# Kernel optimization log

Hardware: AMD Instinct MI355X
Metric: run time of the kernel (lower is better)

## Reference

```python
import jax, jax.numpy as jnp
import numpy as np

DIM = 512
HEADS = 8
DHEAD = DIM // HEADS
M = DIM // 2          # num_landmarks = 256
ITERS = 6             # pinv iterations
KSIZE = 33            # residual conv kernel (seq axis)
EPS = 1e-5            # LayerNorm eps (torch default)


def moore_penrose_pinv(a, iters=ITERS):
    # a: [b, h, m, m]; iterative Newton-Schulz style pseudo-inverse
    abs_a = jnp.abs(a)
    col = abs_a.sum(-1).max()   # global max of row-sums
    row = abs_a.sum(-2).max()   # global max of col-sums
    z = jnp.swapaxes(a, -1, -2) / (col * row)
    I = jnp.eye(a.shape[-1], dtype=a.dtype)

    def body(z, _):
        az = a @ z
        z = 0.25 * z @ (13.0 * I - az @ (15.0 * I - az @ (7.0 * I - az)))
        return z, None

    z, _ = jax.lax.scan(body, z, None, length=iters)
    return z


def res_conv(v, conv_w):
    # v: [b, h, n, d] treated as NCHW (C=heads), depthwise kernel (33, 1)
    return jax.lax.conv_general_dilated(
        v, conv_w, window_strides=(1, 1),
        padding=((KSIZE // 2, KSIZE // 2), (0, 0)),
        dimension_numbers=('NCHW', 'OIHW', 'NCHW'),
        feature_group_count=HEADS)


def setup_inputs() -> dict:
    key = jax.random.key(0)
    ks = jax.random.split(key, 5)
    b, n = 4, 4096  # n % M == 0 -> no padding branch
    x = jax.random.normal(ks[0], (b, n, DIM), jnp.float32)
    norm_w = jnp.ones((DIM,), jnp.float32)
    norm_b = jnp.zeros((DIM,), jnp.float32)
    Wqkv = jax.random.normal(ks[1], (DIM, 3 * DIM), jnp.float32) * (DIM ** -0.5)
    Wout = jax.random.normal(ks[2], (DIM, DIM), jnp.float32) * (DIM ** -0.5)
    bout = jnp.zeros((DIM,), jnp.float32)
    conv_w = jax.random.normal(ks[3], (HEADS, 1, KSIZE, 1), jnp.float32) * 0.05
    return {"x": x, "norm_w": norm_w, "norm_b": norm_b,
            "Wqkv": Wqkv, "Wout": Wout, "bout": bout, "conv_w": conv_w}


def reference(x, norm_w, norm_b, Wqkv, Wout, bout, conv_w):
    b, n, dim = x.shape
    # LayerNorm
    mu = x.mean(-1, keepdims=True)
    var = ((x - mu) ** 2).mean(-1, keepdims=True)
    xn = (x - mu) * jax.lax.rsqrt(var + EPS) * norm_w + norm_b

    # QKV projection, split heads: [b, h, n, d]
    qkv = xn @ Wqkv
    q, k, v = jnp.split(qkv, 3, axis=-1)
    sh = lambda t: t.reshape(b, n, HEADS, DHEAD).transpose(0, 2, 1, 3)
    q, k, v = sh(q), sh(k), sh(v)
    q = q * (DHEAD ** -0.5)

    # landmarks: mean over consecutive segments of length l = n // M
    l = n // M
    q_l = q.reshape(b, HEADS, M, l, DHEAD).mean(3)  # [b,h,m,d]
    k_l = k.reshape(b, HEADS, M, l, DHEAD).mean(3)

    sim1 = jnp.einsum('bhid,bhjd->bhij', q, k_l)    # [b,h,n,m]
    sim2 = jnp.einsum('bhid,bhjd->bhij', q_l, k_l)  # [b,h,m,m]
    sim3 = jnp.einsum('bhid,bhjd->bhij', q_l, k)    # [b,h,m,n]
    a1 = jax.nn.softmax(sim1, axis=-1)
    a2 = jax.nn.softmax(sim2, axis=-1)
    a3 = jax.nn.softmax(sim3, axis=-1)

    a2_inv = moore_penrose_pinv(a2)
    out = (a1 @ a2_inv) @ (a3 @ v)                  # [b,h,n,d]
    out = out + res_conv(v, conv_w)                  # residual depthwise conv on v

    out = out.transpose(0, 2, 1, 3).reshape(b, n, dim)
    out = out @ Wout + bout                          # to_out (dropout = identity in eval)
    return x + out                                   # TransLayer residual
```

## Files before the change

kernel.cpp:

```cpp
#include <hip/hip_runtime.h>
#include <hip/hip_bf16.h>

#define BB 4
#define NN 4096
#define DIMM 512
#define HH 8
#define DD 64
#define MM 256
#define LL 16
#define BHH 32
#define NROW (BB*NN)
#define KS 33

typedef __attribute__((ext_vector_type(8))) short short8;
typedef __attribute__((ext_vector_type(4))) float float4v;

static __device__ __forceinline__ unsigned short bf16_bits(float v) {
    __hip_bfloat16 h = __float2bfloat16(v);
    return *reinterpret_cast<unsigned short*>(&h);
}

static __device__ __forceinline__ void gl_lds16(const void* g, void* l) {
    __builtin_amdgcn_global_load_lds((const __attribute__((address_space(1))) void*)g,
                                     (__attribute__((address_space(3))) void*)l, 16, 0, 0);
}

static __device__ __forceinline__ void bar_nv() {
    asm volatile("s_waitcnt lgkmcnt(0)\ns_barrier" ::: "memory");
}

static __device__ __forceinline__ int xcd_swz(int hw, int nwg) {
    return (hw & 7) * (nwg >> 3) + (hw >> 3);
}

__launch_bounds__(256)
__global__ void ln_kernel(const float* __restrict__ x,
                          const float* __restrict__ w,
                          const float* __restrict__ bvec,
                          __hip_bfloat16* __restrict__ xn) {
    int row = blockIdx.x;
    int t = threadIdx.x;
    const float* xr = x + (long)row * DIMM;
    float v0 = xr[t];
    float v1 = xr[t + 256];
    __shared__ float red[256];
    red[t] = v0 + v1;
    __syncthreads();
    for (int off = 128; off > 0; off >>= 1) { if (t < off) red[t] += red[t + off]; __syncthreads(); }
    float mu = red[0] * (1.0f / DIMM);
    __syncthreads();
    float d0 = v0 - mu, d1 = v1 - mu;
    red[t] = d0 * d0 + d1 * d1;
    __syncthreads();
    for (int off = 128; off > 0; off >>= 1) { if (t < off) red[t] += red[t + off]; __syncthreads(); }
    float var = red[0] * (1.0f / DIMM);
    float rs = rsqrtf(var + 1e-5f);
    xn[(long)row * DIMM + t]       = __float2bfloat16(d0 * rs * w[t]       + bvec[t]);
    xn[(long)row * DIMM + t + 256] = __float2bfloat16(d1 * rs * w[t + 256] + bvec[t + 256]);
}

__launch_bounds__(256)
__global__ void transpose_bf16(const float* __restrict__ in, __hip_bfloat16* __restrict__ outp,
                               int K, int N) {
    __shared__ float tile[32][33];
    int k0 = blockIdx.y * 32, n0 = blockIdx.x * 32;
    int tx = threadIdx.x & 31, ty = threadIdx.x >> 5;
    #pragma unroll
    for (int i = 0; i < 32; i += 8)
        tile[ty + i][tx] = in[(long)(k0 + ty + i) * N + n0 + tx];
    __syncthreads();
    #pragma unroll
    for (int i = 0; i < 32; i += 8)
        outp[(long)(n0 + ty + i) * K + k0 + tx] = __float2bfloat16(tile[tx][ty + i]);
}

enum { EPI_NONE = 0, EPI_QKV = 1, EPI_OUT = 2 };

template<int EPI>
__launch_bounds__(256)
__global__ void gemm_mfma(const __hip_bfloat16* __restrict__ A,
                          const __hip_bfloat16* __restrict__ Bt,
                          float* __restrict__ C, int M, int N, int K,
                          const float* __restrict__ bias,
                          const float* __restrict__ resid,
                          __hip_bfloat16* __restrict__ qb,
                          __hip_bfloat16* __restrict__ kb,
                          __hip_bfloat16* __restrict__ vtb) {
    __shared__ __hip_bfloat16 As[128][64];
    __shared__ __hip_bfloat16 Bs[128][64];
    const int t = threadIdx.x;
    const int hw = blockIdx.y * gridDim.x + blockIdx.x;
    const int lg = xcd_swz(hw, gridDim.x * gridDim.y);
    const int m0 = (lg / gridDim.x) * 128, n0 = (lg % gridDim.x) * 128;
    const int wave = t >> 6, lane = t & 63;
    const int wrow = wave >> 1, wcol = wave & 1;
    const int lm = lane & 15, quad = lane >> 4;
    const int wbase = wave * 64;

    const __hip_bfloat16* gA[4];
    const __hip_bfloat16* gB[4];
    __hip_bfloat16* lA[4];
    __hip_bfloat16* lB[4];
    #pragma unroll
    for (int p = 0; p < 4; ++p) {
        int idx = t + p * 256;
        int r = idx >> 3;
// ... 53 lines not shown
        for (int j = 0; j < 4; ++j) {
            int rowb = m0 + wrow * 64 + i * 16 + quad * 4;
            int col  = n0 + wcol * 64 + j * 16 + lm;
            if (EPI == EPI_QKV) {
                int b = rowb >> 12, seq = rowb & (NN - 1);
                int which = col >> 9, rem = col & 511;
                int h = rem >> 6, dd = rem & 63;
                int bh = b * HH + h;
                if (which == 0) {
                    #pragma unroll
                    for (int r = 0; r < 4; ++r)
                        qb[((long)bh * NN + seq + r) * DD + dd] = __float2bfloat16(acc[i][j][r] * 0.125f);
                } else if (which == 1) {
                    #pragma unroll
                    for (int r = 0; r < 4; ++r)
                        kb[((long)bh * NN + seq + r) * DD + dd] = __float2bfloat16(acc[i][j][r]);
                } else {
                    union { unsigned long long u; unsigned short s[4]; } pk;
                    #pragma unroll
                    for (int r = 0; r < 4; ++r) pk.s[r] = bf16_bits(acc[i][j][r]);
                    *(unsigned long long*)&vtb[((long)bh * DD + dd) * NN + seq] = pk.u;
                }
            } else {
                #pragma unroll
                for (int r = 0; r < 4; ++r) {
                    int row = rowb + r;
                    C[(long)row * N + col] = acc[i][j][r] + bias[col] + resid[(long)row * N + col];
                }
            }
        }
    }
}

__launch_bounds__(256)
__global__ void gemm_pinv(const __hip_bfloat16* __restrict__ A,
                          const __hip_bfloat16* __restrict__ Bt,
                          __hip_bfloat16* __restrict__ CnBf,
                          float* __restrict__ CnF,
                          __hip_bfloat16* __restrict__ CTbf,
                          float diag, float sgn, float scale) {
    __shared__ __hip_bfloat16 As[64][256];
    __shared__ __hip_bfloat16 Bs[64][256];
    const int t = threadIdx.x;
    const int hw = (blockIdx.z * 4 + blockIdx.y) * 4 + blockIdx.x;
    const int lg = xcd_swz(hw, 512);
    const long base = (long)(lg >> 4) << 16;
    const int m0 = ((lg >> 2) & 3) * 64, n0 = (lg & 3) * 64;
    const int wave = t >> 6, lane = t & 63;
    const int wr = wave >> 1, wc = wave & 1;
    const int lm = lane & 15, quad = lane >> 4;
    const __hip_bfloat16* Ab = A + base;
    const __hip_bfloat16* Bb = Bt + base;

    #pragma unroll
    for (int p = 0; p < 8; ++p) {
        int idx = t + p * 256;
        int r = idx >> 5;
        int csrc = ((idx & 31) ^ (r & 7)) * 8;
        int cb = idx * 8;
        gl_lds16(&Ab[(long)(m0 + r) * 256 + csrc], &As[0][0] + cb);
        gl_lds16(&Bb[(long)(n0 + r) * 256 + csrc], &Bs[0][0] + cb);
    }

    const char* pA[2][2];
    const char* pB[2][2];
    #pragma unroll
    for (int i = 0; i < 2; ++i) {
        int ra = wr * 32 + i * 16 + lm;
        int rb = wc * 32 + i * 16 + lm;
        int ca = quad ^ (ra & 3), ra2 = (ra >> 2) & 1;
        int cb2 = quad ^ (rb & 3), rb2 = (rb >> 2) & 1;
        pA[0][i] = (const char*)&As[ra][(4 * ra2       + ca)  * 8];
        pA[1][i] = (const char*)&As[ra][(4 * (1 - ra2) + ca)  * 8];
        pB[0][i] = (const char*)&Bs[rb][(4 * rb2       + cb2) * 8];
        pB[1][i] = (const char*)&Bs[rb][(4 * (1 - rb2) + cb2) * 8];
    }
    __syncthreads();

// ... 4 lines not shown
        #pragma unroll
        for (int i = 0; i < 2; ++i) {
            af[i]  = *(const short8*)(pA[ksu & 1][i] + (ksu >> 1) * 128);
            bfr[i] = *(const short8*)(pB[ksu & 1][i] + (ksu >> 1) * 128);
        }
        #pragma unroll
        for (int i = 0; i < 2; ++i)
            #pragma unroll
            for (int j = 0; j < 2; ++j)
                acc[i][j] = __builtin_amdgcn_mfma_f32_16x16x32_bf16(af[i], bfr[j], acc[i][j], 0, 0, 0);
    }

    #pragma unroll
    for (int i = 0; i < 2; ++i)
        #pragma unroll
        for (int j = 0; j < 2; ++j) {
            const int rowb = wr * 32 + i * 16 + quad * 4;
            const int col  = wc * 32 + j * 16 + lm;
            union { unsigned long long u; unsigned short s[4]; } pk;
            #pragma unroll
            for (int r = 0; r < 4; ++r) {
                float v = acc[i][j][r] * scale;
                long off = base + (long)(m0 + rowb + r) * 256 + n0 + col;
                if (CnBf) CnBf[off] = __float2bfloat16(v);
                if (CnF)  CnF[off]  = v;
                float tv = sgn * v + ((m0 + rowb + r) == (n0 + col) ? diag : 0.0f);
                pk.s[r] = bf16_bits(tv);
            }
            if (CTbf)
                *(unsigned long long*)&CTbf[base + (long)(n0 + col) * 256 + m0 + rowb] = pk.u;
        }
}

__launch_bounds__(256)
__global__ void gemm_pinv2(const __hip_bfloat16* __restrict__ zA,
                           const __hip_bfloat16* __restrict__ pAg,
                           const __hip_bfloat16* __restrict__ t3T,
                           __hip_bfloat16* __restrict__ zOut,
                           float* __restrict__ zF,
                           __hip_bfloat16* __restrict__ pOut,
                           __hip_bfloat16* __restrict__ t1T) {
    __shared__ __hip_bfloat16 As[64][256];
    __shared__ __hip_bfloat16 Bs[64][256];
    const int t = threadIdx.x;
    const int hw = blockIdx.y * 16 + blockIdx.x;
    const int lg = xcd_swz(hw, 1024);
    const int pair = lg >> 5;
    const int half = (lg >> 4) & 1;
    const int tile = lg & 15;
    const long base = (long)pair << 16;
    const int m0 = (tile >> 2) * 64, n0 = (tile & 3) * 64;
    const int wave = t >> 6, lane = t & 63;
    const int wr = wave >> 1, wc = wave & 1;
    const int lm = lane & 15, quad = lane >> 4;
    const __hip_bfloat16* Ab = (half ? pAg : zA) + base;
    const __hip_bfloat16* Bb = t3T + base;

    #pragma unroll
    for (int p = 0; p < 8; ++p) {
        int idx = t + p * 256;
        int r = idx >> 5;
        int csrc = ((idx & 31) ^ (r & 7)) * 8;
        int cb = idx * 8;
        gl_lds16(&Ab[(long)(m0 + r) * 256 + csrc], &As[0][0] + cb);
        gl_lds16(&Bb[(long)(n0 + r) * 256 + csrc], &Bs[0][0] + cb);
    }

    const char* pA[2][2];
    const char* pB[2][2];
    #pragma unroll
    for (int i = 0; i < 2; ++i) {
        int ra = wr * 32 + i * 16 + lm;
        int rb = wc * 32 + i * 16 + lm;
        int ca = quad ^ (ra & 3), ra2 = (ra >> 2) & 1;
        int cb2 = quad ^ (rb & 3), rb2 = (rb >> 2) & 1;
        pA[0][i] = (const char*)&As[ra][(4 * ra2       + ca)  * 8];
// ... 15 lines not shown
        #pragma unroll
        for (int i = 0; i < 2; ++i)
            #pragma unroll
            for (int j = 0; j < 2; ++j)
                acc[i][j] = __builtin_amdgcn_mfma_f32_16x16x32_bf16(af[i], bfr[j], acc[i][j], 0, 0, 0);
    }

    #pragma unroll
    for (int i = 0; i < 2; ++i)
        #pragma unroll
        for (int j = 0; j < 2; ++j) {
            const int rowb = wr * 32 + i * 16 + quad * 4;
            const int col  = wc * 32 + j * 16 + lm;
            union { unsigned long long u; unsigned short s[4]; } pk;
            #pragma unroll
            for (int r = 0; r < 4; ++r) {
                float v = acc[i][j][r] * 0.25f;
                long off = base + (long)(m0 + rowb + r) * 256 + n0 + col;
                if (half == 0) {
                    zOut[off] = __float2bfloat16(v);
                    if (zF) zF[off] = v;
                } else {
                    pOut[off] = __float2bfloat16(v);
                    float tv = -v + ((m0 + rowb + r) == (n0 + col) ? 7.0f : 0.0f);
                    pk.s[r] = bf16_bits(tv);
                }
            }
            if (half)
                *(unsigned long long*)&t1T[base + (long)(n0 + col) * 256 + m0 + rowb] = pk.u;
        }
}

__launch_bounds__(256)
__global__ void pinv_prep(const float* __restrict__ a2, const float* __restrict__ scl,
                          __hip_bfloat16* __restrict__ a2bf, __hip_bfloat16* __restrict__ z0T,
                          __hip_bfloat16* __restrict__ z0n) {
    __shared__ float tl[64][65];
    const int t = threadIdx.x;
    const long base = (long)blockIdx.z << 16;
    const int i0 = blockIdx.y * 64, j0 = blockIdx.x * 64;
    float s = scl[0];
    #pragma unroll
    for (int p = 0; p < 16; ++p) {
        int idx = t + p * 256;
        int r = idx >> 6, c = idx & 63;
        long off = base + (long)(i0 + r) * 256 + j0 + c;
        float v = a2[off];
        a2bf[off] = __float2bfloat16(v);
        float zv = v * s;
        z0T[off] = __float2bfloat16(zv);
        tl[r][c] = zv;
    }
    __syncthreads();
    int r = t & 63;
    #pragma unroll
    for (int u = 0; u < 16; ++u) {
        int c = u * 4 + (t >> 6);
        z0n[base + (long)(j0 + c) * 256 + i0 + r] = __float2bfloat16(tl[r][c]);
    }
}

__launch_bounds__(256)
__global__ void sim2_softmax(const float* __restrict__ q_l, const float* __restrict__ k_l,
                             float* __restrict__ a2) {
    const int t = threadIdx.x;
    const int lg = xcd_swz(blockIdx.x, 128);
    const int bh = lg >> 2;
    const int m0 = (lg & 3) * 64;
    const int tx = t & 15, ty = t >> 4;
    const float* Ab = q_l + (long)bh * MM * DD;
    const float* Bb = k_l + (long)bh * MM * DD;

    __shared__ float As[16][64];
    __shared__ float Bs[16][256];

    float acc[4][16] = {};

    for (int k0 = 0; k0 < DD; k0 += 16) {
        {
            int r = t >> 2, kk4 = (t & 3) * 4;
            float4 va = *(const float4*)(Ab + (long)(m0 + r) * DD + k0 + kk4);
            As[kk4 + 0][r] = va.x; As[kk4 + 1][r] = va.y; As[kk4 + 2][r] = va.z; As[kk4 + 3][r] = va.w;
        }
        {
            #pragma unroll
            for (int g = 0; g < 4; ++g) {
                float4 vb = *(const float4*)(Bb + (long)t * DD + k0 + g * 4);
                Bs[g * 4 + 0][t] = vb.x; Bs[g * 4 + 1][t] = vb.y;
                Bs[g * 4 + 2][t] = vb.z; Bs[g * 4 + 3][t] = vb.w;
            }
        }
        __syncthreads();
        #pragma unroll
        for (int kk = 0; kk < 16; ++kk) {
            float a[4], b[16];
            #pragma unroll
            for (int r2 = 0; r2 < 4; ++r2) a[r2] = As[kk][ty * 4 + r2];
            #pragma unroll
// ... 7 lines not shown
        __syncthreads();
    }

    float* outb = a2 + ((long)bh << 16);
    #pragma unroll
    for (int r2 = 0; r2 < 4; ++r2) {
        float mx = acc[r2][0];
        #pragma unroll
        for (int c = 1; c < 16; ++c) mx = fmaxf(mx, acc[r2][c]);
        mx = fmaxf(mx, __shfl_xor(mx, 1));
        mx = fmaxf(mx, __shfl_xor(mx, 2));
        mx = fmaxf(mx, __shfl_xor(mx, 4));
        mx = fmaxf(mx, __shfl_xor(mx, 8));
        float sum = 0.f;
        #pragma unroll
        for (int c = 0; c < 16; ++c) {
            acc[r2][c] = __expf(acc[r2][c] - mx);
            sum += acc[r2][c];
        }
        sum += __shfl_xor(sum, 1);
        sum += __shfl_xor(sum, 2);
        sum += __shfl_xor(sum, 4);
        sum += __shfl_xor(sum, 8);
        float inv = 1.0f / sum;
        int row = m0 + ty * 4 + r2;
        #pragma unroll
        for (int c = 0; c < 16; ++c)
            outb[(long)row * 256 + tx + 16 * c] = acc[r2][c] * inv;
    }
}

__launch_bounds__(256)
__global__ void gemm64(const float* __restrict__ A, const float* __restrict__ Bm,
                       float* __restrict__ C, __hip_bfloat16* __restrict__ wtT,
                       int M, int N, int K, long sA, long sB, long sC, float alpha) {
    const int gx = gridDim.x, gxy = gridDim.x * gridDim.y;
    const int hw = blockIdx.z * gxy + blockIdx.y * gx + blockIdx.x;
    const int lg = xcd_swz(hw, gxy * gridDim.z);
    const int bz = lg / gxy;
    const int rem = lg % gxy;
    const float* Ab = A + (long)bz * sA;
    const float* Bb = Bm + (long)bz * sB;

    __shared__ float As[16][64];
    __shared__ float Bs[16][64];

    const int tid = threadIdx.x;
    const int tx = tid & 15;
    const int ty = tid >> 4;
    const int m0 = (rem / gx) * 64;
    const int n0 = (rem % gx) * 64;

    float acc[4][4] = {};

    for (int k0 = 0; k0 < K; k0 += 16) {
        {
            int r  = tid >> 2;
            int kk = (tid & 3) * 4;
            float4 va = *(const float4*)(Ab + (long)(m0 + r) * K + k0 + kk);
            As[kk + 0][r] = va.x; As[kk + 1][r] = va.y; As[kk + 2][r] = va.z; As[kk + 3][r] = va.w;
        }
        {
            int kk = tid >> 4;
            int j  = (tid & 15) * 4;
            float4 vb = *(const float4*)(Bb + (long)(k0 + kk) * N + n0 + j);
            Bs[kk][j + 0] = vb.x; Bs[kk][j + 1] = vb.y; Bs[kk][j + 2] = vb.z; Bs[kk][j + 3] = vb.w;
        }
        __syncthreads();
        #pragma unroll
        for (int kk = 0; kk < 16; ++kk) {
            float a0 = As[kk][ty * 4 + 0], a1 = As[kk][ty * 4 + 1];
            float a2 = As[kk][ty * 4 + 2], a3 = As[kk][ty * 4 + 3];
            float b0 = Bs[kk][tx * 4 + 0], b1 = Bs[kk][tx * 4 + 1];
            float b2 = Bs[kk][tx * 4 + 2], b3 = Bs[kk][tx * 4 + 3];
            acc[0][0] += a0 * b0; acc[0][1] += a0 * b1; acc[0][2] += a0 * b2; acc[0][3] += a0 * b3;
            acc[1][0] += a1 * b0; acc[1][1] += a1 * b1; acc[1][2] += a1 * b2; acc[1][3] += a1 * b3;
            acc[2][0] += a2 * b0; acc[2][1] += a2 * b1; acc[2][2] += a2 * b2; acc[2][3] += a2 * b3;
            acc[3][0] += a3 * b0; acc[3][1] += a3 * b1; acc[3][2] += a3 * b2; acc[3][3] += a3 * b3;
        }
        __syncthreads();
    }

    if (wtT) {
        __hip_bfloat16* wb = wtT + (long)bz * DD * MM;
        #pragma unroll
        for (int r = 0; r < 4; ++r)
            #pragma unroll
            for (int c = 0; c < 4; ++c)
                wb[(long)(n0 + tx * 4 + c) * MM + m0 + ty * 4 + r] = __float2bfloat16(acc[r][c] * alpha);
    } else {
        float* Cb = C + (long)bz * sC;
        #pragma unroll
        for (int r = 0; r < 4; ++r)
            #pragma unroll
            for (int c = 0; c < 4; ++c)
                Cb[(long)(m0 + ty * 4 + r) * N + n0 + tx * 4 + c] = acc[r][c] * alpha;
    }
}

__global__ void landmark_kernel(const __hip_bfloat16* __restrict__ qb,
                                const __hip_bfloat16* __restrict__ kb,
                                float* __restrict__ q_l, float* __restrict__ k_l,
                                __hip_bfloat16* __restrict__ q_lb,
                                __hip_bfloat16* __restrict__ k_lb) {
    int bh = blockIdx.x >> 8;
    int m  = blockIdx.x & 255;
    int d  = threadIdx.x;
    const __hip_bfloat16* src = (blockIdx.y ? kb : qb) + ((long)bh * NN + m * LL) * DD + d;
    float s = 0.f;
    #pragma unroll
    for (int t = 0; t < LL; ++t) s += __bfloat162float(src[(long)t * DD]);
    s *= (1.0f / LL);
    long off = ((long)bh * MM + m) * DD + d;
    if (blockIdx.y) { k_l[off] = s; k_lb[off] = __float2bfloat16(s); }
    else            { q_l[off] = s; q_lb[off] = __float2bfloat16(s); }
}

__launch_bounds__(256)
__global__ void redmax_kernel(const float* __restrict__ a2, float* __restrict__ red) {
    int blk = blockIdx.x;
    int bh = blk >> 3, cg = blk & 7;
    int t = threadIdx.x;
    const float* Ab = a2 + ((long)bh << 16) + cg * 32;
    int c = t & 31, rg = t >> 5;
    float s = 0.f;
    for (int r = rg * 32; r < rg * 32 + 32; ++r) s += Ab[(long)r * 256 + c];
    __shared__ float m[256];
    m[t] = s;
    __syncthreads();
    if (t < 32) {
        float cs = 0.f;
        #pragma unroll
        for (int g = 0; g < 8; ++g) cs += m[t + 32 * g];
        m[t] = cs;
    }
    __syncthreads();
    if (t == 0) {
        float mx = m[0];
        #pragma unroll
        for (int i = 1; i < 32; ++i) mx = fmaxf(mx, m[i]);
        red[blk] = mx;
    }
}

__launch_bounds__(256)
__global__ void scale_kernel(const float* __restrict__ red, float* __restrict__ scl) {
    __shared__ float b[256];
    int t = threadIdx.x;
    b[t] = red[t];
    __syncthreads();
    for (int off = 128; off > 0; off >>= 1) {
        if (t < off) b[t] = fmaxf(b[t], b[t + off]);
        __syncthreads();
    }
    if (t == 0) scl[0] = 1.0f / b[0];
}

__launch_bounds__(256)
__global__ void a3v_mfma(const __hip_bfloat16* __restrict__ qlb,
                         const __hip_bfloat16* __restrict__ kb,
                         const __hip_bfloat16* __restrict__ vtb,
                         float* __restrict__ opart, float* __restrict__ lpart) {
    const int hw = blockIdx.y * 16 + blockIdx.x;
    const int lg = xcd_swz(hw, 512);
    const int bh = lg >> 4;
    const int mt = (lg >> 2) & 3;
    const int ns = lg & 3;
    const int t = threadIdx.x;
    const int wave = t >> 6, lane = t & 63;
    const int wr = wave >> 1, wc = wave & 1;
    const int lm = lane & 15, quad = lane >> 4;
    const int r8 = t >> 3, c8 = (t & 7) * 8;

    __shared__ __hip_bfloat16 Qs[64][72];
    __shared__ __hip_bfloat16 Ks[64][72];
    __shared__ __hip_bfloat16 Vt[64][72];
    __shared__ __hip_bfloat16 Ps[64][72];
    __shared__ float lredS[64][2];

    {
        const __hip_bfloat16* qbase = qlb + ((long)bh * MM + mt * 64) * DD;
        *(uint4*)&Qs[r8][c8]      = *(const uint4*)&qbase[(long)r8 * DD + c8];
        *(uint4*)&Qs[r8 + 32][c8] = *(const uint4*)&qbase[(long)(r8 + 32) * DD + c8];
    }

    float4v acc[2][2] = {};
    float lacc[2][4] = {};
    const __hip_bfloat16* kbase = kb + ((long)bh * NN + ns * 1024) * DD;
    const __hip_bfloat16* vbase = vtb + (long)bh * DD * NN + ns * 1024;

    uint4 kv0 = *(const uint4*)&kbase[(long)r8 * DD + c8];
    uint4 kv1 = *(const uint4*)&kbase[(long)(r8 + 32) * DD + c8];
    uint4 vv0 = *(const uint4*)&vbase[(long)r8 * NN + c8];
    uint4 vv1 = *(const uint4*)&vbase[(long)(r8 + 32) * NN + c8];
    bar_nv();

    for (int ch = 0; ch < 16; ++ch) {
        *(uint4*)&Ks[r8][c8]      = kv0;
        *(uint4*)&Ks[r8 + 32][c8] = kv1;
        *(uint4*)&Vt[r8][c8]      = vv0;
        *(uint4*)&Vt[r8 + 32][c8] = vv1;
        if (ch < 15) {
            kv0 = *(const uint4*)&kbase[(long)((ch + 1) * 64 + r8) * DD + c8];
            kv1 = *(const uint4*)&kbase[(long)((ch + 1) * 64 + r8 + 32) * DD + c8];
            vv0 = *(const uint4*)&vbase[(long)r8 * NN + (ch + 1) * 64 + c8];
            vv1 = *(const uint4*)&vbase[(long)(r8 + 32) * NN + (ch + 1) * 64 + c8];
        }
        bar_nv();

        float4v s[2][2] = {};
        #pragma unroll
        for (int ks = 0; ks < 64; ks += 32) {
            short8 af[2], bfr[2];
            #pragma unroll
            for (int i = 0; i < 2; ++i) {
                af[i]  = *(const short8*)&Qs[wr * 32 + i * 16 + lm][ks + quad * 8];
                bfr[i] = *(const short8*)&Ks[wc * 32 + i * 16 + lm][ks + quad * 8];
            }
            #pragma unroll
            for (int i = 0; i < 2; ++i)
                #pragma unroll
                for (int j = 0; j < 2; ++j)
                    s[i][j] = __builtin_amdgcn_mfma_f32_16x16x32_bf16(af[i], bfr[j], s[i][j], 0, 0, 0);
        }
        #pragma unroll
        for (int i = 0; i < 2; ++i)
            #pragma unroll
            for (int j = 0; j < 2; ++j)
                #pragma unroll
                for (int r2 = 0; r2 < 4; ++r2) {
                    float e = __expf(s[i][j][r2]);
                    lacc[i][r2] += e;
                    Ps[wr * 32 + i * 16 + quad * 4 + r2][wc * 32 + j * 16 + lm] = __float2bfloat16(e);
                }
        bar_nv();

        #pragma unroll
        for (int ks = 0; ks < 64; ks += 32) {
            short8 af[2], bfr[2];
            #pragma unroll
            for (int i = 0; i < 2; ++i) {
                af[i]  = *(const short8*)&Ps[wr * 32 + i * 16 + lm][ks + quad * 8];
                bfr[i] = *(const short8*)&Vt[wc * 32 + i * 16 + lm][ks + quad * 8];
            }
            #pragma unroll
            for (int i = 0; i < 2; ++i)
                #pragma unroll
                for (int j = 0; j < 2; ++j)
                    acc[i][j] = __builtin_amdgcn_mfma_f32_16x16x32_bf16(af[i], bfr[j], acc[i][j], 0, 0, 0);
        }
        bar_nv();
    }

    #pragma unroll
    for (int i = 0; i < 2; ++i)
        #pragma unroll
        for (int r2 = 0; r2 < 4; ++r2) {
            float s = lacc[i][r2];
            s += __shfl_xor(s, 1);
            s += __shfl_xor(s, 2);
            s += __shfl_xor(s, 4);
            s += __shfl_xor(s, 8);
            if (lm == 0) lredS[wr * 32 + i * 16 + quad * 4 + r2][wc] = s;
        }
    __syncthreads();
    if (t < 64)
        lpart[((bh * 4 + mt) * 4 + ns) * 64 + t] = lredS[t][0] + lredS[t][1];
    const long pbase = ((long)((bh * 4 + mt) * 4 + ns)) << 12;
    #pragma unroll
    for (int i = 0; i < 2; ++i)
        #pragma unroll
        for (int j = 0; j < 2; ++j)
            #pragma unroll
            for (int r2 = 0; r2 < 4; ++r2)
                opart[pbase + (long)(wr * 32 + i * 16 + quad * 4 + r2) * 64 + wc * 32 + j * 16 + lm] = acc[i][j][r2];
}

__global__ void a3v_combine(const float* __restrict__ opart, const float* __restrict__ lpart,
                            float* __restrict__ a3v) {
    int idx = blockIdx.x * 256 + threadIdx.x;
    int d  = idx & 63;
    int m  = (idx >> 6) & 255;
    int bh = idx >> 14;
    int mt = m >> 6, r = m & 63;
    int pb = (bh * 4 + mt) * 4;
    float osum = 0.f, lsum = 0.f;
    #pragma unroll
    for (int ns = 0; ns < 4; ++ns) {
        osum += opart[(((long)(pb + ns)) << 12) + r * 64 + d];
        lsum += lpart[(pb + ns) * 64 + r];
    }
    a3v[((long)bh * MM + m) * DD + d] = osum / lsum;
}

__launch_bounds__(256)
__global__ void attn_out_mfma(const __hip_bfloat16* __restrict__ qb,
                              const __hip_bfloat16* __restrict__ klb,
                              const __hip_bfloat16* __restrict__ wtb,
                              const __hip_bfloat16* __restrict__ vtb,
                              const float* __restrict__ convw,
                              __hip_bfloat16* __restrict__ ctx) {
    const int hw = blockIdx.y * 64 + blockIdx.x;
    const int lg = xcd_swz(hw, 2048);
    const int bh = lg >> 6;
    const int b = bh >> 3, h = bh & 7;
    const int i0 = (lg & 63) * 64;
    const int t = threadIdx.x;
    const int wave = t >> 6, lane = t & 63;
    const int wr = wave >> 1, wc = wave & 1;
    const int lm = lane & 15, quad = lane >> 4;
    const int r8 = t >> 3, c8 = (t & 7) * 8;

    __shared__ __hip_bfloat16 Qs[64][72];
    __shared__ __hip_bfloat16 KW[2][64][72];
    __shared__ __hip_bfloat16 Ps[64][72];
    __shared__ __hip_bfloat16 Vc[64][104];
    __shared__ float lredS[64][2];
    __shared__ float dsum[64];
    __shared__ float cwS[KS];
    __hip_bfloat16 (*Tpl)[104] = reinterpret_cast<__hip_bfloat16 (*)[104]>(&KW[0][0][0]);

    if (t < KS) cwS[t] = convw[h * KS + t];

    {
        const __hip_bfloat16* qbase = qb + ((long)bh * NN + i0) * DD;
// ... 157 lines not shown
    const float* norm_b = (const float*)d_in[2];
    const float* Wqkv   = (const float*)d_in[3];
    const float* Wout   = (const float*)d_in[4];
    const float* bout   = (const float*)d_in[5];
    const float* conv_w = (const float*)d_in[6];
    float* out = (float*)d_out;

    float* ws = (float*)d_ws;
    size_t o = 0;
    auto alloc = [&](size_t n) { float* p = ws + o; o += n; return p; };
    auto allocb = [&](size_t n) { return (__hip_bfloat16*)alloc((n + 1) / 2); };

    __hip_bfloat16* xn_bf  = allocb((size_t)NROW * DIMM);
    __hip_bfloat16* wqt_bf = allocb((size_t)3 * DIMM * DIMM);
    __hip_bfloat16* wot_bf = allocb((size_t)DIMM * DIMM);
    __hip_bfloat16* ctx_bf = allocb((size_t)NROW * DIMM);
    __hip_bfloat16* q_bf   = allocb((size_t)BHH * NN * DD);
    __hip_bfloat16* k_bf   = allocb((size_t)BHH * NN * DD);
    __hip_bfloat16* vt_bf  = allocb((size_t)BHH * DD * NN);
    __hip_bfloat16* qlb    = allocb((size_t)BHH * MM * DD);
    __hip_bfloat16* klb    = allocb((size_t)BHH * MM * DD);
    __hip_bfloat16* wt_bf  = allocb((size_t)BHH * DD * MM);
    float* q_l  = alloc((size_t)BHH * MM * DD);
    float* k_l  = alloc((size_t)BHH * MM * DD);
    float* a2   = alloc((size_t)BHH * MM * MM);
    float* zb   = alloc((size_t)BHH * MM * MM);
    float* az   = alloc((size_t)BHH * MM * MM);
    float* gb   = alloc((size_t)BHH * MM * MM);
    float* tb   = alloc((size_t)BHH * MM * MM);
    float* z2   = alloc((size_t)BHH * MM * MM);
    float* a3v  = alloc((size_t)BHH * MM * DD);
    float* opart = alloc((size_t)BHH * 4 * 4 * 64 * 64);
    float* lpart = alloc((size_t)BHH * 4 * 4 * 64);
    float* red  = alloc(256);
    float* scl  = alloc(64);

    const size_t HB = 1048576;
    __hip_bfloat16* a2bf = (__hip_bfloat16*)az;
    __hip_bfloat16* z0Tb = (__hip_bfloat16*)(az + HB);
    __hip_bfloat16* zpA  = (__hip_bfloat16*)gb;
    __hip_bfloat16* zpB  = (__hip_bfloat16*)(gb + HB);
    __hip_bfloat16* PnA  = (__hip_bfloat16*)tb;
    __hip_bfloat16* t1A  = (__hip_bfloat16*)(tb + HB);
    __hip_bfloat16* t2T  = (__hip_bfloat16*)z2;
    __hip_bfloat16* t3Tb = (__hip_bfloat16*)(z2 + HB);

    ln_kernel<<<NROW, 256, 0, stream>>>(x, norm_w, norm_b, xn_bf);

    transpose_bf16<<<dim3(3 * DIMM / 32, DIMM / 32), 256, 0, stream>>>(Wqkv, wqt_bf, DIMM, 3 * DIMM);
    transpose_bf16<<<dim3(DIMM / 32, DIMM / 32), 256, 0, stream>>>(Wout, wot_bf, DIMM, DIMM);

    gemm_mfma<EPI_QKV><<<dim3(3 * DIMM / 128, NROW / 128), 256, 0, stream>>>(
        xn_bf, wqt_bf, nullptr, NROW, 3 * DIMM, DIMM,
        nullptr, nullptr, q_bf, k_bf, vt_bf);

    landmark_kernel<<<dim3(BHH * MM, 2), 64, 0, stream>>>(q_bf, k_bf, q_l, k_l, qlb, klb);

    sim2_softmax<<<128, 256, 0, stream>>>(q_l, k_l, a2);

    redmax_kernel<<<BHH * 8, 256, 0, stream>>>(a2, red);
    scale_kernel<<<1, 256, 0, stream>>>(red, scl);

    dim3 g512(4, 4, BHH);
    pinv_prep<<<g512, 256, 0, stream>>>(a2, scl, a2bf, z0Tb, zpA);

    gemm_pinv<<<g512, 256, 0, stream>>>(a2bf, z0Tb, PnA, nullptr, t1A, 7.0f, -1.0f, 1.0f);
    __hip_bfloat16 *zi = zpA, *zo = zpB;
    __hip_bfloat16 *Pc = PnA, *Pn2 = a2bf;
    __hip_bfloat16 *t1c = t1A, *t1n = z0Tb;
    for (int it = 0; it < 6; ++it) {
        gemm_pinv<<<g512, 256, 0, stream>>>(Pc, t1c, nullptr, nullptr, t2T, 15.0f, -1.0f, 1.0f);
        gemm_pinv<<<g512, 256, 0, stream>>>(Pc, t2T, nullptr, nullptr, t3Tb, 13.0f, -1.0f, 1.0f);
        gemm_pinv2<<<dim3(16, 64), 256, 0, stream>>>(zi, Pc, t3Tb, zo,
                                                     (it == 5) ? zb : nullptr, Pn2, t1n);
        __hip_bfloat16* tmp;
        tmp = zi; zi = zo; zo = tmp;
        tmp = Pc; Pc = Pn2; Pn2 = tmp;
        tmp = t1c; t1c = t1n; t1n = tmp;
    }

    a3v_mfma<<<dim3(16, BHH), 256, 0, stream>>>(qlb, k_bf, vt_bf, opart, lpart);
    a3v_combine<<<BHH * MM * DD / 256, 256, 0, stream>>>(opart, lpart, a3v);

    gemm64<<<dim3(1, 4, BHH), 256, 0, stream>>>(
        zb, a3v, nullptr, wt_bf, MM, DD, MM, (long)MM * MM, (long)MM * DD, (long)MM * DD, 1.0f);

    attn_out_mfma<<<dim3(NN / 64, BHH), 256, 0, stream>>>(
        q_bf, klb, wt_bf, vt_bf, conv_w, ctx_bf);

    gemm_mfma<EPI_OUT><<<dim3(DIMM / 128, NROW / 128), 256, 0, stream>>>(
        ctx_bf, wot_bf, out, NROW, DIMM, DIMM,
        bout, x, nullptr, nullptr, nullptr);
}
```

Measured before the change: 381.3 us.

## Merge small kernels into combined launches and overlap a3v with pinv

Several small launches are merged into shared kernels. LayerNorm and the two weight transposes run as one launch. The global max reduction uses an atomicMax on float bits, which removes the separate scale kernel. The a3v attention kernel now shares a launch with the first pinv GEMM, and its combine step shares a launch with the next pinv GEMM, so independent work fills idle CUs during the latency-bound pinv chain. This saves launch overhead and serialization, but the merged kernels always reserve 64KB LDS even for the lighter branches, which can lower occupancy. The atomicMax-on-bits trick relies on the values being non-negative.

New measurement: 408.9 us. 1.07x slower.

```diff
diff --git a/kernel.cpp b/kernel.cpp
--- a/kernel.cpp
+++ b/kernel.cpp
@@ -34,44 +34,51 @@
 }
 
 __launch_bounds__(256)
-__global__ void ln_kernel(const float* __restrict__ x,
-                          const float* __restrict__ w,
-                          const float* __restrict__ bvec,
-                          __hip_bfloat16* __restrict__ xn) {
-    int row = blockIdx.x;
-    int t = threadIdx.x;
-    const float* xr = x + (long)row * DIMM;
-    float v0 = xr[t];
-    float v1 = xr[t + 256];
-    __shared__ float red[256];
-    red[t] = v0 + v1;
-    __syncthreads();
-    for (int off = 128; off > 0; off >>= 1) { if (t < off) red[t] += red[t + off]; __syncthreads(); }
-    float mu = red[0] * (1.0f / DIMM);
-    __syncthreads();
-    float d0 = v0 - mu, d1 = v1 - mu;
-    red[t] = d0 * d0 + d1 * d1;
-    __syncthreads();
-    for (int off = 128; off > 0; off >>= 1) { if (t < off) red[t] += red[t + off]; __syncthreads(); }
-    float var = red[0] * (1.0f / DIMM);
-    float rs = rsqrtf(var + 1e-5f);
-    xn[(long)row * DIMM + t]       = __float2bfloat16(d0 * rs * w[t]       + bvec[t]);
-    xn[(long)row * DIMM + t + 256] = __float2bfloat16(d1 * rs * w[t + 256] + bvec[t + 256]);
-}
-
-__launch_bounds__(256)
-__global__ void transpose_bf16(const float* __restrict__ in, __hip_bfloat16* __restrict__ outp,
-                               int K, int N) {
-    __shared__ float tile[32][33];
-    int k0 = blockIdx.y * 32, n0 = blockIdx.x * 32;
-    int tx = threadIdx.x & 31, ty = threadIdx.x >> 5;
-    #pragma unroll
-    for (int i = 0; i < 32; i += 8)
-        tile[ty + i][tx] = in[(long)(k0 + ty + i) * N + n0 + tx];
-    __syncthreads();
-    #pragma unroll
-    for (int i = 0; i < 32; i += 8)
-        outp[(long)(n0 + ty + i) * K + k0 + tx] = __float2bfloat16(tile[tx][ty + i]);
+__global__ void ln_fused(const float* __restrict__ x,
+                         const float* __restrict__ w,
+                         const float* __restrict__ bvec,
+                         __hip_bfloat16* __restrict__ xn,
+                         const float* __restrict__ Wqkv,
+                         __hip_bfloat16* __restrict__ wqt,
+                         const float* __restrict__ Wout,
+                         __hip_bfloat16* __restrict__ wot) {
+    __shared__ __align__(16) char smem[4352];
+    const int t = threadIdx.x;
+    const int hw = blockIdx.x;
+    if (hw < NROW) {
+        float* red = reinterpret_cast<float*>(smem);
+        const float* xr = x + (long)hw * DIMM;
+        float v0 = xr[t];
+        float v1 = xr[t + 256];
+        red[t] = v0 + v1;
+        __syncthreads();
+        for (int off = 128; off > 0; off >>= 1) { if (t < off) red[t] += red[t + off]; __syncthreads(); }
+        float mu = red[0] * (1.0f / DIMM);
+        __syncthreads();
+        float d0 = v0 - mu, d1 = v1 - mu;
+        red[t] = d0 * d0 + d1 * d1;
+        __syncthreads();
+        for (int off = 128; off > 0; off >>= 1) { if (t < off) red[t] += red[t + off]; __syncthreads(); }
+        float var = red[0] * (1.0f / DIMM);
+        float rs = rsqrtf(var + 1e-5f);
+        xn[(long)hw * DIMM + t]       = __float2bfloat16(d0 * rs * w[t]       + bvec[t]);
+        xn[(long)hw * DIMM + t + 256] = __float2bfloat16(d1 * rs * w[t + 256] + bvec[t + 256]);
+    } else {
+        float (*tile)[33] = reinterpret_cast<float (*)[33]>(smem);
+        int idx = hw - NROW;
+        const float* in; __hip_bfloat16* outp; int K, N, bx, by;
+        if (idx < 768) { in = Wqkv; outp = wqt; K = 512; N = 1536; bx = idx % 48; by = idx / 48; }
+        else { idx -= 768; in = Wout; outp = wot; K = 512; N = 512; bx = idx % 16; by = idx / 16; }
+        int k0 = by * 32, n0 = bx * 32;
+        int tx = t & 31, ty = t >> 5;
+        #pragma unroll
+        for (int i = 0; i < 32; i += 8)
+            tile[ty + i][tx] = in[(long)(k0 + ty + i) * N + n0 + tx];
+        __syncthreads();
+        #pragma unroll
+        for (int i = 0; i < 32; i += 8)
+            outp[(long)(n0 + ty + i) * K + k0 + tx] = __float2bfloat16(tile[tx][ty + i]);
+    }
 }
 
 enum { EPI_NONE = 0, EPI_QKV = 1, EPI_OUT = 2 };
@@ -191,18 +198,13 @@
     }
 }
 
-__launch_bounds__(256)
-__global__ void gemm_pinv(const __hip_bfloat16* __restrict__ A,
-                          const __hip_bfloat16* __restrict__ Bt,
-                          __hip_bfloat16* __restrict__ CnBf,
-                          float* __restrict__ CnF,
-                          __hip_bfloat16* __restrict__ CTbf,
-                          float diag, float sgn, float scale) {
-    __shared__ __hip_bfloat16 As[64][256];
-    __shared__ __hip_bfloat16 Bs[64][256];
-    const int t = threadIdx.x;
-    const int hw = (blockIdx.z * 4 + blockIdx.y) * 4 + blockIdx.x;
-    const int lg = xcd_swz(hw, 512);
+static __device__ __forceinline__ void pinv_tile_run(
+    const __hip_bfloat16* __restrict__ A, const __hip_bfloat16* __restrict__ Bt,
+    __hip_bfloat16* CnBf, float* CnF, __hip_bfloat16* CTbf,
+    float diag, float sgn, float scale, int lg, char* smem, int t)
+{
+    __hip_bfloat16 (*As)[256] = reinterpret_cast<__hip_bfloat16 (*)[256]>(smem);
+    __hip_bfloat16 (*Bs)[256] = reinterpret_cast<__hip_bfloat16 (*)[256]>(smem + 32768);
     const long base = (long)(lg >> 4) << 16;
     const int m0 = ((lg >> 2) & 3) * 64, n0 = (lg & 3) * 64;
     const int wave = t >> 6, lane = t & 63;
@@ -273,6 +275,182 @@
         }
 }
 
+static __device__ __forceinline__ void a3v_run(
+    const __hip_bfloat16* __restrict__ qlb, const __hip_bfloat16* __restrict__ kb,
+    const __hip_bfloat16* __restrict__ vtb,
+    float* __restrict__ opart, float* __restrict__ lpart,
+    int lg, char* smem, int t)
+{
+    __hip_bfloat16 (*Qs)[72] = reinterpret_cast<__hip_bfloat16 (*)[72]>(smem);
+    __hip_bfloat16 (*Ks)[72] = reinterpret_cast<__hip_bfloat16 (*)[72]>(smem + 9216);
+    __hip_bfloat16 (*Vt)[72] = reinterpret_cast<__hip_bfloat16 (*)[72]>(smem + 18432);
+    __hip_bfloat16 (*Ps)[72] = reinterpret_cast<__hip_bfloat16 (*)[72]>(smem + 27648);
+    float (*lredS)[2] = reinterpret_cast<float (*)[2]>(smem + 36864);
+    const int bh = lg >> 4;
+    const int mt = (lg >> 2) & 3;
+    const int ns = lg & 3;
+    const int wave = t >> 6, lane = t & 63;
+    const int wr = wave >> 1, wc = wave & 1;
+    const int lm = lane & 15, quad = lane >> 4;
+    const int r8 = t >> 3, c8 = (t & 7) * 8;
+
+    {
+        const __hip_bfloat16* qbase = qlb + ((long)bh * MM + mt * 64) * DD;
+        *(uint4*)&Qs[r8][c8]      = *(const uint4*)&qbase[(long)r8 * DD + c8];
+        *(uint4*)&Qs[r8 + 32][c8] = *(const uint4*)&qbase[(long)(r8 + 32) * DD + c8];
+    }
+
+    float4v acc[2][2] = {};
+    float lacc[2][4] = {};
+    const __hip_bfloat16* kbase = kb + ((long)bh * NN + ns * 1024) * DD;
+    const __hip_bfloat16* vbase = vtb + (long)bh * DD * NN + ns * 1024;
+
+    uint4 kv0 = *(const uint4*)&kbase[(long)r8 * DD + c8];
+    uint4 kv1 = *(const uint4*)&kbase[(long)(r8 + 32) * DD + c8];
+    uint4 vv0 = *(const uint4*)&vbase[(long)r8 * NN + c8];
+    uint4 vv1 = *(const uint4*)&vbase[(long)(r8 + 32) * NN + c8];
+    bar_nv();
+
+    for (int ch = 0; ch < 16; ++ch) {
+        *(uint4*)&Ks[r8][c8]      = kv0;
+        *(uint4*)&Ks[r8 + 32][c8] = kv1;
+        *(uint4*)&Vt[r8][c8]      = vv0;
+        *(uint4*)&Vt[r8 + 32][c8] = vv1;
+        if (ch < 15) {
+            kv0 = *(const uint4*)&kbase[(long)((ch + 1) * 64 + r8) * DD + c8];
+            kv1 = *(const uint4*)&kbase[(long)((ch + 1) * 64 + r8 + 32) * DD + c8];
+            vv0 = *(const uint4*)&vbase[(long)r8 * NN + (ch + 1) * 64 + c8];
+            vv1 = *(const uint4*)&vbase[(long)(r8 + 32) * NN + (ch + 1) * 64 + c8];
+        }
+        bar_nv();
+
+        float4v s[2][2] = {};
+        #pragma unroll
+        for (int ks = 0; ks < 64; ks += 32) {
+            short8 af[2], bfr[2];
+            #pragma unroll
+            for (int i = 0; i < 2; ++i) {
+                af[i]  = *(const short8*)&Qs[wr * 32 + i * 16 + lm][ks + quad * 8];
+                bfr[i] = *(const short8*)&Ks[wc * 32 + i * 16 + lm][ks + quad * 8];
+            }
+            #pragma unroll
+            for (int i = 0; i < 2; ++i)
+                #pragma unroll
+                for (int j = 0; j < 2; ++j)
+                    s[i][j] = __builtin_amdgcn_mfma_f32_16x16x32_bf16(af[i], bfr[j], s[i][j], 0, 0, 0);
+        }
+        #pragma unroll
+        for (int i = 0; i < 2; ++i)
+            #pragma unroll
+            for (int j = 0; j < 2; ++j)
+                #pragma unroll
+                for (int r2 = 0; r2 < 4; ++r2) {
+                    float e = __expf(s[i][j][r2]);
+                    lacc[i][r2] += e;
+                    Ps[wr * 32 + i * 16 + quad * 4 + r2][wc * 32 + j * 16 + lm] = __float2bfloat16(e);
+                }
+        bar_nv();
+
+        #pragma unroll
+        for (int ks = 0; ks < 64; ks += 32) {
+            short8 af[2], bfr[2];
+            #pragma unroll
+            for (int i = 0; i < 2; ++i) {
+                af[i]  = *(const short8*)&Ps[wr * 32 + i * 16 + lm][ks + quad * 8];
+                bfr[i] = *(const short8*)&Vt[wc * 32 + i * 16 + lm][ks + quad * 8];
+            }
+            #pragma unroll
+            for (int i = 0; i < 2; ++i)
+                #pragma unroll
+                for (int j = 0; j < 2; ++j)
+                    acc[i][j] = __builtin_amdgcn_mfma_f32_16x16x32_bf16(af[i], bfr[j], acc[i][j], 0, 0, 0);
+        }
+        bar_nv();
+    }
+
+    #pragma unroll
+    for (int i = 0; i < 2; ++i)
+        #pragma unroll
+        for (int r2 = 0; r2 < 4; ++r2) {
+            float s = lacc[i][r2];
+            s += __shfl_xor(s, 1);
+            s += __shfl_xor(s, 2);
+            s += __shfl_xor(s, 4);
+            s += __shfl_xor(s, 8);
+            if (lm == 0) lredS[wr * 32 + i * 16 + quad * 4 + r2][wc] = s;
+        }
+    __syncthreads();
+    if (t < 64)
+        lpart[((bh * 4 + mt) * 4 + ns) * 64 + t] = lredS[t][0] + lredS[t][1];
+    const long pbase = ((long)((bh * 4 + mt) * 4 + ns)) << 12;
+    #pragma unroll
+    for (int i = 0; i < 2; ++i)
+        #pragma unroll
+        for (int j = 0; j < 2; ++j)
+            #pragma unroll
+            for (int r2 = 0; r2 < 4; ++r2)
+                opart[pbase + (long)(wr * 32 + i * 16 + quad * 4 + r2) * 64 + wc * 32 + j * 16 + lm] = acc[i][j][r2];
+}
+
+__launch_bounds__(256)
+__global__ void gemm_pinv(const __hip_bfloat16* __restrict__ A,
+                          const __hip_bfloat16* __restrict__ Bt,
+                          __hip_bfloat16* __restrict__ CnBf,
+                          float* __restrict__ CnF,
+                          __hip_bfloat16* __restrict__ CTbf,
+                          float diag, float sgn, float scale) {
+    __shared__ __align__(16) char smem[65536];
+    const int hw = blockIdx.x;
+    const int lg = xcd_swz(hw, 512);
+    pinv_tile_run(A, Bt, CnBf, CnF, CTbf, diag, sgn, scale, lg, smem, threadIdx.x);
+}
+
+__launch_bounds__(256)
+__global__ void pinv_p0_a3v(const __hip_bfloat16* __restrict__ a2bf,
+                            const __hip_bfloat16* __restrict__ z0T,
+                            __hip_bfloat16* __restrict__ P0,
+                            __hip_bfloat16* __restrict__ t1T,
+                            const __hip_bfloat16* __restrict__ qlb,
+                            const __hip_bfloat16* __restrict__ kb,
+                            const __hip_bfloat16* __restrict__ vtb,
+                            float* __restrict__ opart, float* __restrict__ lpart) {
+    __shared__ __align__(16) char smem[65536];
+    const int lg = xcd_swz(blockIdx.x, 1024);
+    if (lg < 512)
+        pinv_tile_run(a2bf, z0T, P0, nullptr, t1T, 7.0f, -1.0f, 1.0f, lg, smem, threadIdx.x);
+    else
+        a3v_run(qlb, kb, vtb, opart, lpart, lg - 512, smem, threadIdx.x);
+}
+
+__launch_bounds__(256)
+__global__ void pinv_t2_comb(const __hip_bfloat16* __restrict__ P,
+                             const __hip_bfloat16* __restrict__ t1T,
+                             __hip_bfloat16* __restrict__ t2T,
+                             const float* __restrict__ opart,
+                             const float* __restrict__ lpart,
+                             float* __restrict__ a3v) {
+    __shared__ __align__(16) char smem[65536];
+    const int t = threadIdx.x;
+    const int lg = xcd_swz(blockIdx.x, 2560);
+    if (lg < 512) {
+        pinv_tile_run(P, t1T, nullptr, nullptr, t2T, 15.0f, -1.0f, 1.0f, lg, smem, t);
+    } else {
+        int idx = (lg - 512) * 256 + t;
+        int d  = idx & 63;
+        int m  = (idx >> 6) & 255;
+        int bh = idx >> 14;
+        int mt = m >> 6, r = m & 63;
+        int pb = (bh * 4 + mt) * 4;
+        float osum = 0.f, lsum = 0.f;
+        #pragma unroll
+        for (int ns = 0; ns < 4; ++ns) {
+            osum += opart[(((long)(pb + ns)) << 12) + r * 64 + d];
+            lsum += lpart[(pb + ns) * 64 + r];
+        }
+        a3v[((long)bh * MM + m) * DD + d] = osum / lsum;
+    }
+}
+
 __launch_bounds__(256)
 __global__ void gemm_pinv2(const __hip_bfloat16* __restrict__ zA,
                            const __hip_bfloat16* __restrict__ pAg,
@@ -281,8 +459,9 @@
                            float* __restrict__ zF,
                            __hip_bfloat16* __restrict__ pOut,
                            __hip_bfloat16* __restrict__ t1T) {
-    __shared__ __hip_bfloat16 As[64][256];
-    __shared__ __hip_bfloat16 Bs[64][256];
+    __shared__ __align__(16) char smem[65536];
+    __hip_bfloat16 (*As)[256] = reinterpret_cast<__hip_bfloat16 (*)[256]>(smem);
+    __hip_bfloat16 (*Bs)[256] = reinterpret_cast<__hip_bfloat16 (*)[256]>(smem + 32768);
     const int t = threadIdx.x;
     const int hw = blockIdx.y * 16 + blockIdx.x;
     const int lg = xcd_swz(hw, 1024);
@@ -364,14 +543,14 @@
 }
 
 __launch_bounds__(256)
-__global__ void pinv_prep(const float* __restrict__ a2, const float* __restrict__ scl,
+__global__ void pinv_prep(const float* __restrict__ a2, const unsigned* __restrict__ sclraw,
                           __hip_bfloat16* __restrict__ a2bf, __hip_bfloat16* __restrict__ z0T,
                           __hip_bfloat16* __restrict__ z0n) {
     __shared__ float tl[64][65];
     const int t = threadIdx.x;
     const long base = (long)blockIdx.z << 16;
     const int i0 = blockIdx.y * 64, j0 = blockIdx.x * 64;
-    float s = scl[0];
+    float s = 1.0f / __uint_as_float(sclraw[0]);
     #pragma unroll
     for (int p = 0; p < 16; ++p) {
         int idx = t + p * 256;
@@ -394,8 +573,9 @@
 
 __launch_bounds__(256)
 __global__ void sim2_softmax(const float* __restrict__ q_l, const float* __restrict__ k_l,
-                             float* __restrict__ a2) {
+                             float* __restrict__ a2, unsigned* __restrict__ sclraw) {
     const int t = threadIdx.x;
+    if (blockIdx.x == 0 && t == 0) sclraw[0] = 0u;
     const int lg = xcd_swz(blockIdx.x, 128);
     const int bh = lg >> 2;
     const int m0 = (lg & 3) * 64;
@@ -469,8 +649,8 @@
 
 __launch_bounds__(256)
 __global__ void gemm64(const float* __restrict__ A, const float* __restrict__ Bm,
-                       float* __restrict__ C, __hip_bfloat16* __restrict__ wtT,
-                       int M, int N, int K, long sA, long sB, long sC, float alpha) {
+                       __hip_bfloat16* __restrict__ wtT,
+                       int M, int N, int K, long sA, long sB, float alpha) {
     const int gx = gridDim.x, gxy = gridDim.x * gridDim.y;
     const int hw = blockIdx.z * gxy + blockIdx.y * gx + blockIdx.x;
     const int lg = xcd_swz(hw, gxy * gridDim.z);
@@ -518,21 +698,12 @@
         __syncthreads();
     }
 
-    if (wtT) {
-        __hip_bfloat16* wb = wtT + (long)bz * DD * MM;
-        #pragma unroll
-        for (int r = 0; r < 4; ++r)
-            #pragma unroll
-            for (int c = 0; c < 4; ++c)
-                wb[(long)(n0 + tx * 4 + c) * MM + m0 + ty * 4 + r] = __float2bfloat16(acc[r][c] * alpha);
-    } else {
-        float* Cb = C + (long)bz * sC;
-        #pragma unroll
-        for (int r = 0; r < 4; ++r)
-            #pragma unroll
-            for (int c = 0; c < 4; ++c)
-                Cb[(long)(m0 + ty * 4 + r) * N + n0 + tx * 4 + c] = acc[r][c] * alpha;
-    }
+    __hip_bfloat16* wb = wtT + (long)bz * DD * MM;
+    #pragma unroll
+    for (int r = 0; r < 4; ++r)
+        #pragma unroll
+        for (int c = 0; c < 4; ++c)
+            wb[(long)(n0 + tx * 4 + c) * MM + m0 + ty * 4 + r] = __float2bfloat16(acc[r][c] * alpha);
 }
 
 __global__ void landmark_kernel(const __hip_bfloat16* __restrict__ qb,
@@ -554,7 +725,7 @@
 }
 
 __launch_bounds__(256)
-__global__ void redmax_kernel(const float* __restrict__ a2, float* __restrict__ red) {
+__global__ void redmax_kernel(const float* __restrict__ a2, unsigned* __restrict__ sclraw) {
     int blk = blockIdx.x;
     int bh = blk >> 3, cg = blk & 7;
     int t = threadIdx.x;
@@ -576,158 +747,8 @@
         float mx = m[0];
         #pragma unroll
         for (int i = 1; i < 32; ++i) mx = fmaxf(mx, m[i]);
-        red[blk] = mx;
-    }
-}
-
-__launch_bounds__(256)
-__global__ void scale_kernel(const float* __restrict__ red, float* __restrict__ scl) {
-    __shared__ float b[256];
-    int t = threadIdx.x;
-    b[t] = red[t];
-    __syncthreads();
-    for (int off = 128; off > 0; off >>= 1) {
-        if (t < off) b[t] = fmaxf(b[t], b[t + off]);
-        __syncthreads();
-    }
-    if (t == 0) scl[0] = 1.0f / b[0];
-}
-
-__launch_bounds__(256)
-__global__ void a3v_mfma(const __hip_bfloat16* __restrict__ qlb,
-                         const __hip_bfloat16* __restrict__ kb,
-                         const __hip_bfloat16* __restrict__ vtb,
-                         float* __restrict__ opart, float* __restrict__ lpart) {
-    const int hw = blockIdx.y * 16 + blockIdx.x;
-    const int lg = xcd_swz(hw, 512);
-    const int bh = lg >> 4;
-    const int mt = (lg >> 2) & 3;
-    const int ns = lg & 3;
-    const int t = threadIdx.x;
-    const int wave = t >> 6, lane = t & 63;
-    const int wr = wave >> 1, wc = wave & 1;
-    const int lm = lane & 15, quad = lane >> 4;
-    const int r8 = t >> 3, c8 = (t & 7) * 8;
-
-    __shared__ __hip_bfloat16 Qs[64][72];
-    __shared__ __hip_bfloat16 Ks[64][72];
-    __shared__ __hip_bfloat16 Vt[64][72];
-    __shared__ __hip_bfloat16 Ps[64][72];
-    __shared__ float lredS[64][2];
-
-    {
-        const __hip_bfloat16* qbase = qlb + ((long)bh * MM + mt * 64) * DD;
-        *(uint4*)&Qs[r8][c8]      = *(const uint4*)&qbase[(long)r8 * DD + c8];
-        *(uint4*)&Qs[r8 + 32][c8] = *(const uint4*)&qbase[(long)(r8 + 32) * DD + c8];
-    }
-
-    float4v acc[2][2] = {};
-    float lacc[2][4] = {};
-    const __hip_bfloat16* kbase = kb + ((long)bh * NN + ns * 1024) * DD;
-    const __hip_bfloat16* vbase = vtb + (long)bh * DD * NN + ns * 1024;
-
-    uint4 kv0 = *(const uint4*)&kbase[(long)r8 * DD + c8];
-    uint4 kv1 = *(const uint4*)&kbase[(long)(r8 + 32) * DD + c8];
-    uint4 vv0 = *(const uint4*)&vbase[(long)r8 * NN + c8];
-    uint4 vv1 = *(const uint4*)&vbase[(long)(r8 + 32) * NN + c8];
-    bar_nv();
-
-    for (int ch = 0; ch < 16; ++ch) {
-        *(uint4*)&Ks[r8][c8]      = kv0;
-        *(uint4*)&Ks[r8 + 32][c8] = kv1;
-        *(uint4*)&Vt[r8][c8]      = vv0;
-        *(uint4*)&Vt[r8 + 32][c8] = vv1;
-        if (ch < 15) {
-            kv0 = *(const uint4*)&kbase[(long)((ch + 1) * 64 + r8) * DD + c8];
-            kv1 = *(const uint4*)&kbase[(long)((ch + 1) * 64 + r8 + 32) * DD + c8];
-            vv0 = *(const uint4*)&vbase[(long)r8 * NN + (ch + 1) * 64 + c8];
-            vv1 = *(const uint4*)&vbase[(long)(r8 + 32) * NN + (ch + 1) * 64 + c8];
-        }
-        bar_nv();
-
-        float4v s[2][2] = {};
-        #pragma unroll
-        for (int ks = 0; ks < 64; ks += 32) {
-            short8 af[2], bfr[2];
-            #pragma unroll
-            for (int i = 0; i < 2; ++i) {
-                af[i]  = *(const short8*)&Qs[wr * 32 + i * 16 + lm][ks + quad * 8];
-                bfr[i] = *(const short8*)&Ks[wc * 32 + i * 16 + lm][ks + quad * 8];
-            }
-            #pragma unroll
-            for (int i = 0; i < 2; ++i)
-                #pragma unroll
-                for (int j = 0; j < 2; ++j)
-                    s[i][j] = __builtin_amdgcn_mfma_f32_16x16x32_bf16(af[i], bfr[j], s[i][j], 0, 0, 0);
-        }
-        #pragma unroll
-        for (int i = 0; i < 2; ++i)
-            #pragma unroll
-            for (int j = 0; j < 2; ++j)
-                #pragma unroll
-                for (int r2 = 0; r2 < 4; ++r2) {
-                    float e = __expf(s[i][j][r2]);
-                    lacc[i][r2] += e;
-                    Ps[wr * 32 + i * 16 + quad * 4 + r2][wc * 32 + j * 16 + lm] = __float2bfloat16(e);
-                }
-        bar_nv();
-
-        #pragma unroll
-        for (int ks = 0; ks < 64; ks += 32) {
-            short8 af[2], bfr[2];
-            #pragma unroll
-            for (int i = 0; i < 2; ++i) {
-                af[i]  = *(const short8*)&Ps[wr * 32 + i * 16 + lm][ks + quad * 8];
-                bfr[i] = *(const short8*)&Vt[wc * 32 + i * 16 + lm][ks + quad * 8];
-            }
-            #pragma unroll
-            for (int i = 0; i < 2; ++i)
-                #pragma unroll
-                for (int j = 0; j < 2; ++j)
-                    acc[i][j] = __builtin_amdgcn_mfma_f32_16x16x32_bf16(af[i], bfr[j], acc[i][j], 0, 0, 0);
-        }
-        bar_nv();
-    }
-
-    #pragma unroll
-    for (int i = 0; i < 2; ++i)
-        #pragma unroll
-        for (int r2 = 0; r2 < 4; ++r2) {
-            float s = lacc[i][r2];
-            s += __shfl_xor(s, 1);
-            s += __shfl_xor(s, 2);
-            s += __shfl_xor(s, 4);
-            s += __shfl_xor(s, 8);
-            if (lm == 0) lredS[wr * 32 + i * 16 + quad * 4 + r2][wc] = s;
-        }
-    __syncthreads();
-    if (t < 64)
-        lpart[((bh * 4 + mt) * 4 + ns) * 64 + t] = lredS[t][0] + lredS[t][1];
-    const long pbase = ((long)((bh * 4 + mt) * 4 + ns)) << 12;
-    #pragma unroll
-    for (int i = 0; i < 2; ++i)
-        #pragma unroll
-        for (int j = 0; j < 2; ++j)
-            #pragma unroll
-            for (int r2 = 0; r2 < 4; ++r2)
-                opart[pbase + (long)(wr * 32 + i * 16 + quad * 4 + r2) * 64 + wc * 32 + j * 16 + lm] = acc[i][j][r2];
-}
-
-__global__ void a3v_combine(const float* __restrict__ opart, const float* __restrict__ lpart,
-                            float* __restrict__ a3v) {
-    int idx = blockIdx.x * 256 + threadIdx.x;
-    int d  = idx & 63;
-    int m  = (idx >> 6) & 255;
-    int bh = idx >> 14;
-    int mt = m >> 6, r = m & 63;
-    int pb = (bh * 4 + mt) * 4;
-    float osum = 0.f, lsum = 0.f;
-    #pragma unroll
-    for (int ns = 0; ns < 4; ++ns) {
-        osum += opart[(((long)(pb + ns)) << 12) + r * 64 + d];
-        lsum += lpart[(pb + ns) * 64 + r];
-    }
-    a3v[((long)bh * MM + m) * DD + d] = osum / lsum;
+        atomicMax(sclraw, __float_as_uint(mx));
+    }
 }
 
 __launch_bounds__(256)
@@ -951,8 +972,7 @@
     float* a3v  = alloc((size_t)BHH * MM * DD);
     float* opart = alloc((size_t)BHH * 4 * 4 * 64 * 64);
     float* lpart = alloc((size_t)BHH * 4 * 4 * 64);
-    float* red  = alloc(256);
-    float* scl  = alloc(64);
+    unsigned* sclraw = (unsigned*)alloc(64);
 
     const size_t HB = 1048576;
     __hip_bfloat16* a2bf = (__hip_bfloat16*)az;
@@ -964,10 +984,8 @@
     __hip_bfloat16* t2T  = (__hip_bfloat16*)z2;
     __hip_bfloat16* t3Tb = (__hip_bfloat16*)(z2 + HB);
 
-    ln_kernel<<<NROW, 256, 0, stream>>>(x, norm_w, norm_b, xn_bf);
-
-    transpose_bf16<<<dim3(3 * DIMM / 32, DIMM / 32), 256, 0, stream>>>(Wqkv, wqt_bf, DIMM, 3 * DIMM);
-    transpose_bf16<<<dim3(DIMM / 32, DIMM / 32), 256, 0, stream>>>(Wout, wot_bf, DIMM, DIMM);
+    ln_fused<<<NROW + 768 + 256, 256, 0, stream>>>(
+        x, norm_w, norm_b, xn_bf, Wqkv, wqt_bf, Wout, wot_bf);
 
     gemm_mfma<EPI_QKV><<<dim3(3 * DIMM / 128, NROW / 128), 256, 0, stream>>>(
         xn_bf, wqt_bf, nullptr, NROW, 3 * DIMM, DIMM,
@@ -975,21 +993,23 @@
 
     landmark_kernel<<<dim3(BHH * MM, 2), 64, 0, stream>>>(q_bf, k_bf, q_l, k_l, qlb, klb);
 
-    sim2_softmax<<<128, 256, 0, stream>>>(q_l, k_l, a2);
-
-    redmax_kernel<<<BHH * 8, 256, 0, stream>>>(a2, red);
-    scale_kernel<<<1, 256, 0, stream>>>(red, scl);
-
-    dim3 g512(4, 4, BHH);
-    pinv_prep<<<g512, 256, 0, stream>>>(a2, scl, a2bf, z0Tb, zpA);
-
-    gemm_pinv<<<g512, 256, 0, stream>>>(a2bf, z0Tb, PnA, nullptr, t1A, 7.0f, -1.0f, 1.0f);
+    sim2_softmax<<<128, 256, 0, stream>>>(q_l, k_l, a2, sclraw);
+
+    redmax_kernel<<<BHH * 8, 256, 0, stream>>>(a2, sclraw);
+
+    pinv_prep<<<dim3(4, 4, BHH), 256, 0, stream>>>(a2, sclraw, a2bf, z0Tb, zpA);
+
+    pinv_p0_a3v<<<1024, 256, 0, stream>>>(a2bf, z0Tb, PnA, t1A,
+                                          qlb, k_bf, vt_bf, opart, lpart);
     __hip_bfloat16 *zi = zpA, *zo = zpB;
     __hip_bfloat16 *Pc = PnA, *Pn2 = a2bf;
     __hip_bfloat16 *t1c = t1A, *t1n = z0Tb;
     for (int it = 0; it < 6; ++it) {
-        gemm_pinv<<<g512, 256, 0, stream>>>(Pc, t1c, nullptr, nullptr, t2T, 15.0f, -1.0f, 1.0f);
-        gemm_pinv<<<g512, 256, 0, stream>>>(Pc, t2T, nullptr, nullptr, t3Tb, 13.0f, -1.0f, 1.0f);
+        if (it == 0)
+            pinv_t2_comb<<<2560, 256, 0, stream>>>(Pc, t1c, t2T, opart, lpart, a3v);
+        else
+            gemm_pinv<<<512, 256, 0, stream>>>(Pc, t1c, nullptr, nullptr, t2T, 15.0f, -1.0f, 1.0f);
+        gemm_pinv<<<512, 256, 0, stream>>>(Pc, t2T, nullptr, nullptr, t3Tb, 13.0f, -1.0f, 1.0f);
         gemm_pinv2<<<dim3(16, 64), 256, 0, stream>>>(zi, Pc, t3Tb, zo,
                                                      (it == 5) ? zb : nullptr, Pn2, t1n);
         __hip_bfloat16* tmp;
@@ -998,11 +1018,8 @@
         tmp = t1c; t1c = t1n; t1n = tmp;
     }
 
-    a3v_mfma<<<dim3(16, BHH), 256, 0, stream>>>(qlb, k_bf, vt_bf, opart, lpart);
-    a3v_combine<<<BHH * MM * DD / 256, 256, 0, stream>>>(opart, lpart, a3v);
-
     gemm64<<<dim3(1, 4, BHH), 256, 0, stream>>>(
-        zb, a3v, nullptr, wt_bf, MM, DD, MM, (long)MM * MM, (long)MM * DD, (long)MM * DD, 1.0f);
+        zb, a3v, wt_bf, MM, DD, MM, (long)MM * MM, (long)MM * DD, 1.0f);
 
     attn_out_mfma<<<dim3(NN / 64, BHH), 256, 0, stream>>>(
         q_bf, klb, wt_bf, vt_bf, conv_w, ctx_bf);
```
